# Optimization experiments

Hardware: AMD Instinct MI355X
Metric: run time of the kernel (lower is better)

Reference implementation:

```python
import jax, jax.numpy as jnp
import numpy as np

B, S, H, NH = 2, 2048, 4096, 32
D = H // NH  # head_dim = 128
ROPE_THETA = 10000.0


def setup_inputs() -> dict:
    key = jax.random.key(0)
    k0, k1, k2 = jax.random.split(key, 3)
    hidden_states = jax.random.normal(k0, (B, S, H), dtype=jnp.float32) * 0.02
    w_pack = jax.random.normal(k1, (H, 3 * H), dtype=jnp.float32) * 0.02  # fused QKV weight
    w_o = jax.random.normal(k2, (H, H), dtype=jnp.float32) * 0.02         # o_proj weight
    positions = jnp.broadcast_to(jnp.arange(S, dtype=jnp.int32), (B, S))
    return {"positions": positions, "hidden_states": hidden_states, "w_pack": w_pack, "w_o": w_o}


def _rope(x, positions):
    # neox-style rotary embedding (vLLM get_rope default), x: [B, S, NH, D]
    half = D // 2
    inv_freq = 1.0 / (ROPE_THETA ** (jnp.arange(0, half, dtype=jnp.float32) * 2.0 / D))
    freqs = positions.astype(jnp.float32)[..., None] * inv_freq  # [B, S, half]
    cos = jnp.cos(freqs)[:, :, None, :]  # [B, S, 1, half]
    sin = jnp.sin(freqs)[:, :, None, :]
    x1, x2 = x[..., :half], x[..., half:]
    return jnp.concatenate([x1 * cos - x2 * sin, x2 * cos + x1 * sin], axis=-1)


def reference(positions, hidden_states, w_pack, w_o):
    # fused QKV projection
    qkv = jnp.einsum('bsh,hf->bsf', hidden_states, w_pack)
    q, k, v = jnp.split(qkv, 3, axis=-1)
    q = q.reshape(B, S, NH, D)
    k = k.reshape(B, S, NH, D)
    v = v.reshape(B, S, NH, D)
    # RoPE on q, k
    q = _rope(q, positions)
    k = _rope(k, positions)
    # causal scaled dot-product attention
    scale = D ** -0.5
    scores = jnp.einsum('bqhd,bkhd->bhqk', q, k) * scale  # [B, NH, S, S]
    causal = jnp.tril(jnp.ones((S, S), dtype=bool))
    scores = jnp.where(causal[None, None], scores, jnp.finfo(scores.dtype).min)
    probs = jax.nn.softmax(scores, axis=-1)
    out = jnp.einsum('bhqk,bkhd->bqhd', probs, v).reshape(B, S, H)
    # output projection
    return jnp.einsum('bsh,hf->bsf', out, w_o)
```

## Files before the change

### kernel.cpp

```cpp
#include <hip/hip_runtime.h>

#define Sdim   2048
#define Hdim   4096
#define NHEADS 32
#define Dh     128
#define Mrows  4096
#define QKVLD  12288

typedef __attribute__((ext_vector_type(8))) short short8;
typedef __attribute__((ext_vector_type(4))) float f32x4;
typedef __attribute__((ext_vector_type(4))) float float4v;

__device__ __forceinline__ short f2bf(float f) {
  union { float f; unsigned u; } x; x.f = f;
  unsigned r = x.u + 0x7fffu + ((x.u >> 16) & 1u);
  return (short)(r >> 16);
}
__device__ __forceinline__ float bf2f(short s) {
  union { unsigned u; float f; } x; x.u = ((unsigned)(unsigned short)s) << 16;
  return x.f;
}

__device__ __forceinline__ void gload_lds16(const void* g, void* l) {
  __builtin_amdgcn_global_load_lds(
      (const __attribute__((address_space(1))) void*)g,
      (__attribute__((address_space(3))) void*)l, 16, 0, 0);
}

__global__ void k_cvt(const float* __restrict__ src, short* __restrict__ dst, int n8) {
  int idx = blockIdx.x * blockDim.x + threadIdx.x;
  if (idx >= n8) return;
  const float4v* s = (const float4v*)src + (size_t)idx * 2;
  float4v a = s[0], b = s[1];
  short8 o;
  o[0] = f2bf(a.x); o[1] = f2bf(a.y); o[2] = f2bf(a.z); o[3] = f2bf(a.w);
  o[4] = f2bf(b.x); o[5] = f2bf(b.y); o[6] = f2bf(b.z); o[7] = f2bf(b.w);
  *((short8*)dst + idx) = o;
}

__global__ void k_transpose_cvt(const float* __restrict__ src, short* __restrict__ dst,
                                int R, int C) {
  __shared__ float tile[32][33];
  int tx = threadIdx.x, ty = threadIdx.y;
  int c0 = blockIdx.x * 32, r0 = blockIdx.y * 32;
#pragma unroll
  for (int j = 0; j < 32; j += 8)
    tile[ty + j][tx] = src[(size_t)(r0 + ty + j) * C + (c0 + tx)];
  __syncthreads();
#pragma unroll
  for (int j = 0; j < 32; j += 8)
    dst[(size_t)(c0 + ty + j) * R + (r0 + tx)] = f2bf(tile[tx][ty + j]);
}

__global__ void k_vt(const short* __restrict__ qkv, short* __restrict__ vt) {
  __shared__ short tile[32][33];
  int tx = threadIdx.x, ty = threadIdx.y;
  int hc0 = blockIdx.x * 32;
  int s0  = blockIdx.y * 32;
  int b   = blockIdx.z;
#pragma unroll
  for (int j = 0; j < 32; j += 8)
    tile[ty + j][tx] = qkv[(size_t)(b * 2048 + s0 + ty + j) * QKVLD + 8192 + hc0 + tx];
  __syncthreads();
#pragma unroll
  for (int j = 0; j < 32; j += 8)
    vt[(size_t)(b * 4096 + hc0 + ty + j) * Sdim + s0 + tx] = tile[tx][ty + j];
}

__device__ __forceinline__ void stage_half256(const short* G, int ld, int row0, int kcol,
                                              char* lds, int tid) {
#pragma unroll
  for (int j = 0; j < 2; ++j) {
    int p = j * 512 + tid;
    int r = p >> 3;
    int c = ((p & 7) ^ (r & 7)) << 3;
    gload_lds16(G + (size_t)(row0 + r) * ld + kcol + c,
                lds + ((j * 512 + (tid & 448)) << 4));
  }
}

#define MFMA_Q(qm, qn)                                                                   \
  do {                                                                                   \
    __builtin_amdgcn_s_setprio(1);                                                       \
    _Pragma("unroll")                                                                    \
    for (int m4 = 0; m4 < 4; ++m4)                                                       \
      _Pragma("unroll")                                                                  \
      for (int n2 = 0; n2 < 2; ++n2) {                                                   \
        acc[(qm)*4+m4][(qn)*2+n2] = __builtin_amdgcn_mfma_f32_16x16x32_bf16(             \
            av[m4][0], bv[(qn)*2+n2][0], acc[(qm)*4+m4][(qn)*2+n2], 0, 0, 0);            \
        acc[(qm)*4+m4][(qn)*2+n2] = __builtin_amdgcn_mfma_f32_16x16x32_bf16(             \
            av[m4][1], bv[(qn)*2+n2][1], acc[(qm)*4+m4][(qn)*2+n2], 0, 0, 0);            \
      }                                                                                  \
    __builtin_amdgcn_s_setprio(0);                                                       \
  } while (0)

#define PH_BARRIER()                    \
  do {                                  \
    __builtin_amdgcn_s_barrier();       \
    __builtin_amdgcn_sched_barrier(0);  \
  } while (0)

template<bool C_F32>
__global__ __launch_bounds__(512, 2) void k_gemm256(const short* __restrict__ A, int lda,
                                                    const short* __restrict__ Bt, int ldb,
                                                    void* __restrict__ Cp, int ldc,
                                                    int Ndim, int Kdim) {
  __shared__ __align__(16) char smem[131072];
  const int tid  = threadIdx.x;
  const int lane = tid & 63;
  const int wave = tid >> 6;
  const int lo = lane & 15, hi = lane >> 4;
  const int wr = wave >> 2, wc = wave & 3;

  const int nblk = gridDim.x;
  const int lid = (blockIdx.x & 7) * (nblk >> 3) + (blockIdx.x >> 3);
  const int nbn = Ndim >> 8;
  const int bm0 = (lid / nbn) << 8;
  const int bn0 = (lid % nbn) << 8;

  f32x4 acc[8][4];
#pragma unroll
  for (int i = 0; i < 8; ++i)
#pragma unroll
    for (int j = 0; j < 4; ++j) acc[i][j] = (f32x4){0.f, 0.f, 0.f, 0.f};

  short8 av[4][2], bv[4][2];
  const int swz = (lo & 7) << 4;
  const int brow = (wc & 1) * 64;

  stage_half256(Bt, ldb, bn0,       0, smem + 32768,         tid);
  stage_half256(Bt, ldb, bn0 + 128, 0, smem + 32768 + 16384, tid);
  stage_half256(A,  lda, bm0,       0, smem,                 tid);
  stage_half256(A,  lda, bm0 + 128, 0, smem + 16384,         tid);

  const int NK = Kdim >> 6;
  for (int kt = 0; kt < NK; ++kt) {
    const int cur = kt & 1;
    const char* Ab = smem + cur * 65536 + wr * 16384;
    const char* Bb = smem + cur * 65536 + 32768 + (wc >> 1) * 16384;
    char* nA = smem + (cur ^ 1) * 65536;
    char* nB = nA + 32768;
    const int kc = (kt + 1) << 6;
    const bool pf = (kt + 1 < NK);

    if (pf) {
      stage_half256(Bt, ldb, bn0,       kc, nB,         tid);
      stage_half256(Bt, ldb, bn0 + 128, kc, nB + 16384, tid);
      asm volatile("s_waitcnt vmcnt(4)" ::: "memory");
    } else {
      asm volatile("s_waitcnt vmcnt(0)" ::: "memory");
    }
    PH_BARRIER();
#pragma unroll
    for (int m4 = 0; m4 < 4; ++m4)
#pragma unroll
      for (int ks = 0; ks < 2; ++ks)
        av[m4][ks] = *(const short8*)(Ab + (m4 * 16 + lo) * 128 + ((ks * 64 + hi * 16) ^ swz));
#pragma unroll
    for (int ni = 0; ni < 2; ++ni)
#pragma unroll
      for (int ks = 0; ks < 2; ++ks)
        bv[ni][ks] = *(const short8*)(Bb + (brow + ni * 16 + lo) * 128 + ((ks * 64 + hi * 16) ^ swz));
    MFMA_Q(0, 0);
#pragma unroll
    for (int ni = 2; ni < 4; ++ni)
#pragma unroll
      for (int ks = 0; ks < 2; ++ks)
        bv[ni][ks] = *(const short8*)(Bb + (brow + ni * 16 + lo) * 128 + ((ks * 64 + hi * 16) ^ swz));

    if (pf) {
      stage_half256(A, lda, bm0,       kc, nA,         tid);
      stage_half256(A, lda, bm0 + 128, kc, nA + 16384, tid);
    }
    PH_BARRIER();
    MFMA_Q(0, 1);
#pragma unroll
    for (int m4 = 0; m4 < 4; ++m4)
#pragma unroll
      for (int ks = 0; ks < 2; ++ks)
        av[m4][ks] = *(const short8*)(Ab + ((64 + m4 * 16 + lo) * 128) + ((ks * 64 + hi * 16) ^ swz));

    PH_BARRIER();
    MFMA_Q(1, 0);

    PH_BARRIER();
    MFMA_Q(1, 1);
  }

#pragma unroll
  for (int mi = 0; mi < 8; ++mi)
#pragma unroll
    for (int r = 0; r < 4; ++r) {
      int row = bm0 + wr * 128 + mi * 16 + hi * 4 + r;
#pragma unroll
      for (int ni = 0; ni < 4; ++ni) {
        int col = bn0 + wc * 64 + ni * 16 + lo;
        if (C_F32) ((float*)Cp)[(size_t)row * ldc + col] = acc[mi][ni][r];
        else       ((short*)Cp)[(size_t)row * ldc + col] = f2bf(acc[mi][ni][r]);
      }
    }
}

__global__ void k_rope(short* qkv, const int* __restrict__ positions) {
  int idx = blockIdx.x * 256 + threadIdx.x;
  int d = idx & 63;
  int h = (idx >> 6) & 31;
  int row = idx >> 11;
  float pos = (float)positions[row];
  float inv = exp2f((float)d * -0.2076205059304570f);
  float ang = pos * inv;
  float s, c;
  sincosf(ang, &s, &c);
  size_t o = (size_t)row * QKVLD + h * 128 + d;
  float q1 = bf2f(qkv[o]),       q2 = bf2f(qkv[o + 64]);
  qkv[o]        = f2bf(q1 * c - q2 * s);
  qkv[o + 64]   = f2bf(q2 * c + q1 * s);
  float k1 = bf2f(qkv[o + 4096]), k2 = bf2f(qkv[o + 4160]);
  qkv[o + 4096] = f2bf(k1 * c - k2 * s);
  qkv[o + 4160] = f2bf(k2 * c + k1 * s);
}

__device__ __forceinline__ void stage_kv(const short* Kb, const short* Vtb, int kv0,
                                         char* kbuf, char* vbuf, int tid, int wave) {
#pragma unroll
  for (int i = 0; i < 4; ++i) {
    int p = i * 256 + tid;
    int r = p >> 4;
    int c = (p & 15) ^ (r & 7);
    gload_lds16(Kb + (size_t)(kv0 + r) * QKVLD + (c << 3),
                kbuf + ((i * 256 + wave * 64) << 4));
  }
#pragma unroll
  for (int i = 0; i < 4; ++i) {
    int p = i * 256 + tid;
    int r = p >> 3;
    int c = (p & 7) ^ (r & 7);
    gload_lds16(Vtb + (size_t)r * Sdim + kv0 + (c << 3),
                vbuf + ((i * 256 + wave * 64) << 4));
  }
}

__global__ __launch_bounds__(256, 2) void k_attn(short* __restrict__ qkv,
                                                 const short* __restrict__ Vt) {
  __shared__ __align__(16) char smem[81920];
  const int tid  = threadIdx.x;
  const int lane = tid & 63;
  const int wave = tid >> 6;
  const int lo = lane & 15, hi = lane >> 4;

  const int bid = blockIdx.x;
  const int lid = (bid & 7) * 128 + (bid >> 3);
  const int bh = lid >> 4;
  const int qt = 15 - (lid & 15);
  const int b = bh >> 5, h = bh & 31;
  const int q0 = qt << 7;

  short* base = qkv + (size_t)b * Sdim * QKVLD;
  const short* Qb = base + h * Dh;
  const short* Kb = base + Hdim + h * Dh;
  const short* Vtb = Vt + (size_t)(b * 32 + h) * 128 * Sdim;
  const int qrow0 = q0 + wave * 32;

  short* Pw = (short*)(smem + 65536 + wave * 4096);

  short8 qf[2][4];
#pragma unroll
  for (int mi = 0; mi < 2; ++mi)
#pragma unroll
    for (int ks = 0; ks < 4; ++ks)
      qf[mi][ks] = *(const short8*)(Qb + (size_t)(qrow0 + mi * 16 + lo) * QKVLD + ks * 32 + hi * 8);

  f32x4 acc_o[2][9];
  float m_run[2][4];
#pragma unroll
  for (int mi = 0; mi < 2; ++mi) {
#pragma unroll
    for (int nf = 0; nf < 9; ++nf) acc_o[mi][nf] = (f32x4){0.f, 0.f, 0.f, 0.f};
#pragma unroll
    for (int r = 0; r < 4; ++r) m_run[mi][r] = -1e30f;
  }

  short8 vones;
#pragma unroll
  for (int j = 0; j < 8; ++j) vones[j] = (short)0x3F80;

  const float SEXP = 0.088388347648318447f * 1.4426950408889634f;
  const int nkv = (q0 + 128) >> 6;
  const int swz = (lo & 7) << 4;

  stage_kv(Kb, Vtb, 0, smem, smem + 16384, tid, wave);
  __syncthreads();

  int cur = 0;
  for (int kvt = 0; kvt < nkv; ++kvt) {
    const int kv0 = kvt << 6;
    if (kvt + 1 < nkv)
      stage_kv(Kb, Vtb, kv0 + 64, smem + (cur ^ 1) * 32768,
               smem + (cur ^ 1) * 32768 + 16384, tid, wave);

    if (kv0 <= qrow0 + 31) {
      const char* kl = smem + cur * 32768;
      const char* vl = smem + cur * 32768 + 16384;

      f32x4 accs[2][4];
#pragma unroll
      for (int mi = 0; mi < 2; ++mi)
#pragma unroll
        for (int nf = 0; nf < 4; ++nf) accs[mi][nf] = (f32x4){0.f, 0.f, 0.f, 0.f};
#pragma unroll
      for (int ks = 0; ks < 4; ++ks) {
        short8 kf[4];
#pragma unroll
        for (int nf = 0; nf < 4; ++nf) {
          int r = nf * 16 + lo;
          kf[nf] = *(const short8*)(kl + r * 256 + ((ks * 64 + hi * 16) ^ swz));
        }
#pragma unroll
        for (int mi = 0; mi < 2; ++mi)
#pragma unroll
          for (int nf = 0; nf < 4; ++nf)
            accs[mi][nf] = __builtin_amdgcn_mfma_f32_16x16x32_bf16(qf[mi][ks], kf[nf], accs[mi][nf], 0, 0, 0);
      }

      const bool needmask = (kv0 + 63 > qrow0);
      float pmax[2][4];
      bool okall = true;
#pragma unroll
      for (int mi = 0; mi < 2; ++mi) {
#pragma unroll
        for (int r = 0; r < 4; ++r) {
          const int qrow = qrow0 + mi * 16 + hi * 4 + r;
          float tmax = -1e30f;
#pragma unroll
          for (int nf = 0; nf < 4; ++nf) {
            float v = accs[mi][nf][r] * SEXP;
            if (needmask) {
              int col = kv0 + nf * 16 + lo;
              v = (col <= qrow) ? v : -1e30f;
            }
            accs[mi][nf][r] = v;
            tmax = fmaxf(tmax, v);
          }
#pragma unroll
          for (int off = 1; off < 16; off <<= 1)
            tmax = fmaxf(tmax, __shfl_xor(tmax, off, 64));
          pmax[mi][r] = tmax;
          okall = okall && (tmax <= m_run[mi][r] + 8.0f);
        }
      }
      if (!__all(okall)) {
#pragma unroll
        for (int mi = 0; mi < 2; ++mi)
#pragma unroll
          for (int r = 0; r < 4; ++r) {
            float mnew = fmaxf(m_run[mi][r], pmax[mi][r]);
            float alpha = exp2f(m_run[mi][r] - mnew);
            m_run[mi][r] = mnew;
#pragma unroll
            for (int nf = 0; nf < 9; ++nf) acc_o[mi][nf][r] *= alpha;
          }
      }
#pragma unroll
      for (int mi = 0; mi < 2; ++mi)
#pragma unroll
        for (int r = 0; r < 4; ++r) {
          const int prow = mi * 16 + hi * 4 + r;
          const int psw = prow & 7;
#pragma unroll
          for (int nf = 0; nf < 4; ++nf) {
            float p = exp2f(accs[mi][nf][r] - m_run[mi][r]);
            int col = nf * 16 + lo;
            Pw[(prow << 6) + (((col >> 3) ^ psw) << 3) + (col & 7)] = f2bf(p);
          }
        }

#pragma unroll
      for (int ks = 0; ks < 2; ++ks) {
        short8 pf[2];
#pragma unroll
        for (int mi = 0; mi < 2; ++mi) {
          int prow = mi * 16 + lo;
          pf[mi] = *(const short8*)((const char*)Pw + prow * 128 + (((ks * 4 + hi) ^ (prow & 7)) << 4));
        }
#pragma unroll
        for (int nf = 0; nf < 9; ++nf) {
          short8 vf;
          if (nf < 8) {
            int row = nf * 16 + lo;
            vf = *(const short8*)(vl + row * 128 + ((ks * 64 + hi * 16) ^ swz));
          } else {
            vf = vones;
          }
#pragma unroll
          for (int mi = 0; mi < 2; ++mi)
            acc_o[mi][nf] = __builtin_amdgcn_mfma_f32_16x16x32_bf16(pf[mi], vf, acc_o[mi][nf], 0, 0, 0);
        }
      }
    }

    __syncthreads();
    cur ^= 1;
  }

  short* Osm = (short*)smem;
#pragma unroll
  for (int mi = 0; mi < 2; ++mi)
#pragma unroll
    for (int r = 0; r < 4; ++r) {
      float inv = 1.0f / acc_o[mi][8][r];
      int row = wave * 32 + mi * 16 + hi * 4 + r;
#pragma unroll
      for (int nf = 0; nf < 8; ++nf)
        Osm[row * 128 + nf * 16 + lo] = f2bf(acc_o[mi][nf][r] * inv);
    }
  __syncthreads();
  short* Ob = base + h * Dh;
#pragma unroll
  for (int it = 0; it < 8; ++it) {
    int chunk = it * 256 + tid;
    int row = chunk >> 4, c8 = chunk & 15;
    *(short8*)(Ob + (size_t)(q0 + row) * QKVLD + c8 * 8) =
        *(const short8*)(Osm + row * 128 + c8 * 8);
  }
}

extern "C" void kernel_launch(void* const* d_in, const int* in_sizes, int n_in,
                              void* d_out, int out_size, void* d_ws, size_t ws_size,
                              hipStream_t stream) {
  const int*   positions = (const int*)d_in[0];
  const float* hidden    = (const float*)d_in[1];
  const float* w_pack    = (const float*)d_in[2];
  const float* w_o       = (const float*)d_in[3];
  float* out = (float*)d_out;

  char* ws = (char*)d_ws;
  short* Wpt  = (short*)ws;
  short* qkvb = (short*)(ws + (size_t)12288 * 4096 * 2);
  short* Wot  = (short*)ws;
  short* Hbf  = (short*)d_out;
  short* Vtg  = (short*)((char*)d_out + ((size_t)32 << 20));

  k_cvt<<<8192, 256, 0, stream>>>(hidden, Hbf, 4096 * 4096 / 8);
  k_transpose_cvt<<<dim3(12288 / 32, 4096 / 32), dim3(32, 8), 0, stream>>>(w_pack, Wpt, 4096, 12288);
  k_gemm256<false><<<dim3(768), 512, 0, stream>>>(Hbf, 4096, Wpt, 4096, qkvb, QKVLD, 12288, 4096);
  k_rope<<<32768, 256, 0, stream>>>(qkvb, positions);
  k_vt<<<dim3(128, 64, 2), dim3(32, 8), 0, stream>>>(qkvb, Vtg);
  k_attn<<<dim3(1024), 256, 0, stream>>>(qkvb, Vtg);
  k_transpose_cvt<<<dim3(4096 / 32, 4096 / 32), dim3(32, 8), 0, stream>>>(w_o, Wot, 4096, 4096);
  k_gemm256<true><<<dim3(256), 512, 0, stream>>>(qkvb, QKVLD, Wot, 4096, out, 4096, 4096, 4096);
}
```

Baseline: 789.7 us.

## Vectorize weight transpose-convert and RoPE, raise MFMA wave priority in attention

The 32x32 transpose-convert is replaced by a 64x64 tile version that reads float4 and writes 8 bf16 values per thread as one 16-byte store. The RoPE kernel now handles 8 elements per thread with 16-byte loads and stores instead of scalar 2-byte accesses. In the attention kernel, s_setprio raises wave priority around the MFMA blocks. Together these aim to cut memory-transaction overhead in the prep kernels and improve overlap in attention. The 64x65 float LDS tile may cause bank conflicts on the strided column reads.

```diff
diff --git a/kernel.cpp b/kernel.cpp
--- a/kernel.cpp
+++ b/kernel.cpp
@@ -38,18 +38,28 @@
   *((short8*)dst + idx) = o;
 }
 
-__global__ void k_transpose_cvt(const float* __restrict__ src, short* __restrict__ dst,
-                                int R, int C) {
-  __shared__ float tile[32][33];
-  int tx = threadIdx.x, ty = threadIdx.y;
-  int c0 = blockIdx.x * 32, r0 = blockIdx.y * 32;
-#pragma unroll
-  for (int j = 0; j < 32; j += 8)
-    tile[ty + j][tx] = src[(size_t)(r0 + ty + j) * C + (c0 + tx)];
+__global__ void k_tcvt64(const float* __restrict__ src, short* __restrict__ dst,
+                         int R, int C) {
+  __shared__ float t[64][65];
+  const int tid = threadIdx.x;
+  const int r0 = blockIdx.y * 64, c0 = blockIdx.x * 64;
+  const int ir = tid >> 4, ic = (tid & 15) << 2;
+#pragma unroll
+  for (int p = 0; p < 4; ++p) {
+    const float4v v = *(const float4v*)(src + (size_t)(r0 + p * 16 + ir) * C + c0 + ic);
+    t[p * 16 + ir][ic] = v.x; t[p * 16 + ir][ic + 1] = v.y;
+    t[p * 16 + ir][ic + 2] = v.z; t[p * 16 + ir][ic + 3] = v.w;
+  }
   __syncthreads();
-#pragma unroll
-  for (int j = 0; j < 32; j += 8)
-    dst[(size_t)(c0 + ty + j) * R + (r0 + tx)] = f2bf(tile[tx][ty + j]);
+  const int oc = tid >> 3, orr = (tid & 7) << 3;
+#pragma unroll
+  for (int p = 0; p < 2; ++p) {
+    int c = p * 32 + oc;
+    short8 o;
+#pragma unroll
+    for (int j = 0; j < 8; ++j) o[j] = f2bf(t[orr + j][c]);
+    *(short8*)(dst + (size_t)(c0 + c) * R + r0 + orr) = o;
+  }
 }
 
 __global__ void k_vt(const short* __restrict__ qkv, short* __restrict__ vt) {
@@ -201,23 +211,28 @@
     }
 }
 
-__global__ void k_rope(short* qkv, const int* __restrict__ positions) {
+__global__ void k_rope8(short* qkv, const int* __restrict__ positions) {
   int idx = blockIdx.x * 256 + threadIdx.x;
-  int d = idx & 63;
-  int h = (idx >> 6) & 31;
-  int row = idx >> 11;
+  int t = idx & 7;
+  int h = (idx >> 3) & 31;
+  int row = idx >> 8;
   float pos = (float)positions[row];
-  float inv = exp2f((float)d * -0.2076205059304570f);
-  float ang = pos * inv;
-  float s, c;
-  sincosf(ang, &s, &c);
-  size_t o = (size_t)row * QKVLD + h * 128 + d;
-  float q1 = bf2f(qkv[o]),       q2 = bf2f(qkv[o + 64]);
-  qkv[o]        = f2bf(q1 * c - q2 * s);
-  qkv[o + 64]   = f2bf(q2 * c + q1 * s);
-  float k1 = bf2f(qkv[o + 4096]), k2 = bf2f(qkv[o + 4160]);
-  qkv[o + 4096] = f2bf(k1 * c - k2 * s);
-  qkv[o + 4160] = f2bf(k2 * c + k1 * s);
+  size_t o = (size_t)row * QKVLD + h * 128 + t * 8;
+  short8 q1 = *(short8*)(qkv + o),        q2 = *(short8*)(qkv + o + 64);
+  short8 k1 = *(short8*)(qkv + o + 4096), k2 = *(short8*)(qkv + o + 4160);
+#pragma unroll
+  for (int j = 0; j < 8; ++j) {
+    int d = t * 8 + j;
+    float inv = exp2f((float)d * -0.2076205059304570f);
+    float ang = pos * inv, s, c;
+    sincosf(ang, &s, &c);
+    float a1 = bf2f(q1[j]), a2 = bf2f(q2[j]);
+    q1[j] = f2bf(a1 * c - a2 * s); q2[j] = f2bf(a2 * c + a1 * s);
+    float b1 = bf2f(k1[j]), b2 = bf2f(k2[j]);
+    k1[j] = f2bf(b1 * c - b2 * s); k2[j] = f2bf(b2 * c + b1 * s);
+  }
+  *(short8*)(qkv + o) = q1;        *(short8*)(qkv + o + 64) = q2;
+  *(short8*)(qkv + o + 4096) = k1; *(short8*)(qkv + o + 4160) = k2;
 }
 
 __device__ __forceinline__ void stage_kv(const short* Kb, const short* Vtb, int kv0,
@@ -315,11 +330,13 @@
           int r = nf * 16 + lo;
           kf[nf] = *(const short8*)(kl + r * 256 + ((ks * 64 + hi * 16) ^ swz));
         }
+        __builtin_amdgcn_s_setprio(1);
 #pragma unroll
         for (int mi = 0; mi < 2; ++mi)
 #pragma unroll
           for (int nf = 0; nf < 4; ++nf)
             accs[mi][nf] = __builtin_amdgcn_mfma_f32_16x16x32_bf16(qf[mi][ks], kf[nf], accs[mi][nf], 0, 0, 0);
+        __builtin_amdgcn_s_setprio(0);
       }
 
       const bool needmask = (kv0 + 63 > qrow0);
@@ -382,6 +399,7 @@
           int prow = mi * 16 + lo;
           pf[mi] = *(const short8*)((const char*)Pw + prow * 128 + (((ks * 4 + hi) ^ (prow & 7)) << 4));
         }
+        __builtin_amdgcn_s_setprio(1);
 #pragma unroll
         for (int nf = 0; nf < 9; ++nf) {
           short8 vf;
@@ -395,6 +413,7 @@
           for (int mi = 0; mi < 2; ++mi)
             acc_o[mi][nf] = __builtin_amdgcn_mfma_f32_16x16x32_bf16(pf[mi], vf, acc_o[mi][nf], 0, 0, 0);
         }
+        __builtin_amdgcn_s_setprio(0);
       }
     }
 
@@ -441,11 +460,11 @@
   short* Vtg  = (short*)((char*)d_out + ((size_t)32 << 20));
 
   k_cvt<<<8192, 256, 0, stream>>>(hidden, Hbf, 4096 * 4096 / 8);
-  k_transpose_cvt<<<dim3(12288 / 32, 4096 / 32), dim3(32, 8), 0, stream>>>(w_pack, Wpt, 4096, 12288);
+  k_tcvt64<<<dim3(12288 / 64, 4096 / 64), 256, 0, stream>>>(w_pack, Wpt, 4096, 12288);
   k_gemm256<false><<<dim3(768), 512, 0, stream>>>(Hbf, 4096, Wpt, 4096, qkvb, QKVLD, 12288, 4096);
-  k_rope<<<32768, 256, 0, stream>>>(qkvb, positions);
+  k_rope8<<<4096, 256, 0, stream>>>(qkvb, positions);
   k_vt<<<dim3(128, 64, 2), dim3(32, 8), 0, stream>>>(qkvb, Vtg);
   k_attn<<<dim3(1024), 256, 0, stream>>>(qkvb, Vtg);
-  k_transpose_cvt<<<dim3(4096 / 32, 4096 / 32), dim3(32, 8), 0, stream>>>(w_o, Wot, 4096, 4096);
+  k_tcvt64<<<dim3(4096 / 64, 4096 / 64), 256, 0, stream>>>(w_o, Wot, 4096, 4096);
   k_gemm256<true><<<dim3(256), 512, 0, stream>>>(qkvb, QKVLD, Wot, 4096, out, 4096, 4096, 4096);
 }
```

Result: faster. 766.5 us (-2.9%).
